# Optimization experiments

Hardware: AMD Instinct MI355X
Metric: run time of the kernel (lower is better)

## Reference

```python
import jax, jax.numpy as jnp
import numpy as np

N_NODES = 100000
N_EDGES = 1600000
D_IN = 128
D_HID = 64
BN_EPS = 1e-5


def setup_inputs() -> dict:
    key = jax.random.key(0)
    ks = jax.random.split(key, 8)
    x = jax.random.normal(ks[0], (N_NODES, D_IN), dtype=jnp.float32)
    edge_index = jax.random.randint(ks[1], (2, N_EDGES), 0, N_NODES, dtype=jnp.int64)
    # GCNConv1 weight/bias (glorot-ish scale)
    W1 = jax.random.normal(ks[2], (D_IN, D_HID), dtype=jnp.float32) / np.sqrt(D_IN)
    b1 = jnp.zeros((D_HID,), dtype=jnp.float32)
    # BatchNorm1d (eval mode: running stats)
    gamma = jax.random.normal(ks[3], (D_HID,), dtype=jnp.float32) * 0.1 + 1.0
    beta = jax.random.normal(ks[4], (D_HID,), dtype=jnp.float32) * 0.1
    run_mean = jnp.zeros((D_HID,), dtype=jnp.float32)
    run_var = jnp.ones((D_HID,), dtype=jnp.float32)
    # fc1: Linear(2*hidden, 2)
    Wfc = jax.random.normal(ks[5], (2 * D_HID, 2), dtype=jnp.float32) / np.sqrt(2 * D_HID)
    bfc = jnp.zeros((2,), dtype=jnp.float32)
    return {"x": x, "edge_index": edge_index, "W1": W1, "b1": b1,
            "gamma": gamma, "beta": beta, "run_mean": run_mean, "run_var": run_var,
            "Wfc": Wfc, "bfc": bfc}


def gcn_conv(x, edge_index, W, b):
    # PyG GCNConv: add self-loops, symmetric normalization, scatter-add aggregation
    n = x.shape[0]
    loops = jnp.arange(n, dtype=edge_index.dtype)
    row = jnp.concatenate([edge_index[0], loops])  # source nodes
    col = jnp.concatenate([edge_index[1], loops])  # target nodes
    deg = jax.ops.segment_sum(jnp.ones_like(col, dtype=x.dtype), col, num_segments=n)
    dinv = jax.lax.rsqrt(jnp.maximum(deg, 1.0))  # deg >= 1 due to self-loops
    norm = dinv[row] * dinv[col]                 # [E+N]
    h = x @ W                                    # [N, hid]
    msgs = h[row] * norm[:, None]                # gather + scale  [E+N, hid]
    out = jax.ops.segment_sum(msgs, col, num_segments=n)  # scatter-add
    return out + b


def reference(x, edge_index, W1, b1, gamma, beta, run_mean, run_var, Wfc, bfc):
    h = gcn_conv(x, edge_index, W1, b1)
    h = jax.nn.relu(h)
    # dropout(p=0.9) is identity in eval mode
    # BatchNorm1d eval: normalize with running stats
    h = (h - run_mean) * jax.lax.rsqrt(run_var + BN_EPS) * gamma + beta
    h = jax.nn.relu(h)
    # edge gather-concat-linear
    er = jnp.concatenate([h[edge_index[0]], h[edge_index[1]]], axis=1)  # [E, 2*hid]
    return er @ Wfc + bfc  # [E, 2]
```

## Files before the change

### kernel.cpp

```cpp
#include <hip/hip_runtime.h>

#define N_NODES 100000
#define N_EDGES 1600000
#define D_IN 128
#define D_HID 64
#define BN_EPS 1e-5f

#define BUCKET_SHIFT 7
#define BUCKET_W 128
#define N_BUCKETS ((N_NODES + BUCKET_W - 1) / BUCKET_W)
#define BCAP 4096
#define N_BIN_BLOCKS 250
#define EDGES_PER_BLOCK (N_EDGES / N_BIN_BLOCKS)
#define E4_PER_BLOCK (EDGES_PER_BLOCK / 4)

typedef __attribute__((ext_vector_type(8))) short bf16x8;
typedef __attribute__((ext_vector_type(4))) float f32x4;
typedef __attribute__((ext_vector_type(8))) _Float16 f16x8;

__device__ __forceinline__ ushort f2bf(float f) {
    unsigned u = __float_as_uint(f);
    u += 0x7FFF + ((u >> 16) & 1);
    return (ushort)(u >> 16);
}

__global__ __launch_bounds__(1024) void bin_scatter_kernel(const int* __restrict__ row,
                                                           const int* __restrict__ col,
                                                           int* __restrict__ bcursor,
                                                           int* __restrict__ binned) {
    __shared__ int hist[N_BUCKETS];
    __shared__ int lbase[N_BUCKETS];
    const int t = threadIdx.x;
    for (int i = t; i < N_BUCKETS; i += 1024) hist[i] = 0;
    __syncthreads();
    const int e0 = blockIdx.x * EDGES_PER_BLOCK;
    const int4* __restrict__ colv = (const int4*)(col + e0);
    const int4* __restrict__ rowv = (const int4*)(row + e0);
    for (int j4 = t; j4 < E4_PER_BLOCK; j4 += 1024) {
        int4 c = colv[j4];
        atomicAdd(&hist[c.x >> BUCKET_SHIFT], 1);
        atomicAdd(&hist[c.y >> BUCKET_SHIFT], 1);
        atomicAdd(&hist[c.z >> BUCKET_SHIFT], 1);
        atomicAdd(&hist[c.w >> BUCKET_SHIFT], 1);
    }
    __syncthreads();
    for (int i = t; i < N_BUCKETS; i += 1024) {
        int h = hist[i];
        lbase[i] = h ? (i * BCAP + atomicAdd(&bcursor[i], h)) : 0;
        hist[i] = 0;
    }
    __syncthreads();
    for (int j4 = t; j4 < E4_PER_BLOCK; j4 += 1024) {
        int4 c = colv[j4];
        int4 r = rowv[j4];
        int cc[4] = {c.x, c.y, c.z, c.w};
        int rr[4] = {r.x, r.y, r.z, r.w};
        #pragma unroll
        for (int k = 0; k < 4; ++k) {
            int b = cc[k] >> BUCKET_SHIFT;
            int rank = atomicAdd(&hist[b], 1);
            binned[lbase[b] + rank] = ((cc[k] & (BUCKET_W - 1)) << 17) | rr[k];
        }
    }
}

union CsrGemmSh {
    struct { int eb[BCAP]; int cl[BCAP]; } s;
    ushort xb[2][16 * 136];
};
__global__ __launch_bounds__(512) void csr_gemm_kernel(const int* __restrict__ binned,
                                                       const int* __restrict__ bcursor,
                                                       const float* __restrict__ x,
                                                       const float* __restrict__ W,
                                                       int* __restrict__ csr_src,
                                                       int2* __restrict__ rs2,
                                                       float* __restrict__ dinv,
                                                       ushort* __restrict__ h_s) {
    __shared__ CsrGemmSh sh;
    __shared__ int hist[BUCKET_W];
    __shared__ int cursor[BUCKET_W];
    __shared__ float dsh[BUCKET_W];
    const int b = blockIdx.x;
    const int t = threadIdx.x;

    const int l = t & 63;
    const int wv = (t >> 6) & 3;
    const int q = l >> 4;
    const int m = l & 15;
    bf16x8 bf[4];
    {
        const int n = wv * 16 + m;
        #pragma unroll
        for (int s = 0; s < 4; ++s)
            #pragma unroll
            for (int j = 0; j < 8; ++j)
                bf[s][j] = (short)f2bf(W[(32 * s + 8 * q + j) * D_HID + n]);
    }

    if (t < BUCKET_W) hist[t] = 0;
    __syncthreads();
    const int s = b * BCAP;
    const int cnt = bcursor[b];
    const int n4 = (cnt + 3) >> 2;
    const int4* __restrict__ binv = (const int4*)(binned + s);
    for (int i4 = t; i4 < n4; i4 += 512) {
        int4 v = binv[i4];
        int vv[4] = {v.x, v.y, v.z, v.w};
        #pragma unroll
        for (int k = 0; k < 4; ++k) {
            int idx = 4 * i4 + k;
            if (idx < cnt) {
                sh.s.eb[idx] = vv[k];
                atomicAdd(&hist[vv[k] >> 17], 1);
            }
        }
    }
    __syncthreads();
    if (t < BUCKET_W) cursor[t] = hist[t];
    for (int off = 1; off < BUCKET_W; off <<= 1) {
        __syncthreads();
        int add = (t >= off && t < BUCKET_W) ? cursor[t - off] : 0;
        __syncthreads();
        if (t < BUCKET_W) cursor[t] += add;
    }
    __syncthreads();
    int excl = (t < BUCKET_W) ? (cursor[t] - hist[t]) : 0;
    __syncthreads();
    if (t < BUCKET_W) cursor[t] = excl;
    {
        const int node = b * BUCKET_W + t;
        if (t < BUCKET_W) {
            float dn = rsqrtf(1.0f + (float)hist[t]);
            dsh[t] = dn;
            if (node < N_NODES) {
                rs2[node] = make_int2(s + excl, hist[t]);
                dinv[node] = dn;
            }
        }
    }
    __syncthreads();
    for (int i = t; i < cnt; i += 512) {
        int p = sh.s.eb[i];
        int pos = atomicAdd(&cursor[p >> 17], 1);
        sh.s.cl[pos] = p & 0x1FFFF;
    }
    __syncthreads();
    {
        int4* __restrict__ csrv = (int4*)(csr_src + s);
        const int4* __restrict__ clv = (const int4*)sh.s.cl;
        for (int i4 = t; i4 < n4; i4 += 512)
            csrv[i4] = clv[i4];
    }
    __syncthreads();

    const int h = t >> 8;
    const int tt = t & 255;
    #pragma unroll
    for (int rnd = 0; rnd < 4; ++rnd) {
        const int node0 = b * BUCKET_W + rnd * 32 + h * 16;
        __syncthreads();
        for (int i = tt; i < 512; i += 256) {
            int r = i >> 5, c4 = i & 31;
            int nr = node0 + r;
            if (nr >= N_NODES) nr = N_NODES - 1;
            float4 v = *(const float4*)&x[(size_t)nr * D_IN + c4 * 4];
            ushort4 u = make_ushort4(f2bf(v.x), f2bf(v.y), f2bf(v.z), f2bf(v.w));
            *(ushort4*)&sh.xb[h][r * 136 + c4 * 4] = u;
        }
        __syncthreads();
        f32x4 acc = {0.f, 0.f, 0.f, 0.f};
        #pragma unroll
        for (int ks = 0; ks < 4; ++ks) {
            bf16x8 af = *(const bf16x8*)&sh.xb[h][m * 136 + 32 * ks + 8 * q];
            acc = __builtin_amdgcn_mfma_f32_16x16x32_bf16(af, bf[ks], acc, 0, 0, 0);
        }
        #pragma unroll
        for (int r = 0; r < 4; ++r) {
            int node = node0 + q * 4 + r;
            if (node < N_NODES) {
                _Float16 hv = (_Float16)(acc[r] * dsh[node - b * BUCKET_W]);
                h_s[node * D_HID + wv * 16 + m] = __builtin_bit_cast(unsigned short, hv);
            }
        }
    }
}

__global__ __launch_bounds__(256) void aggregate_kernel(const ushort* __restrict__ h_s,
                                                        const float* __restrict__ dinv,
                                                        const int2* __restrict__ rs2,
                                                        const int* __restrict__ csr_src,
                                                        const float* __restrict__ b1,
                                                        const float* __restrict__ gamma,
                                                        const float* __restrict__ beta,
                                                        const float* __restrict__ mean,
                                                        const float* __restrict__ var,
                                                        const float* __restrict__ Wfc,
                                                        float4* __restrict__ uv) {
    const f16x8* __restrict__ hsv = (const f16x8*)h_s;
    const int wvid = (blockIdx.x * 256 + threadIdx.x) >> 6;
    const int lane = threadIdx.x & 63;
    const int oct = lane >> 3;
    const int ol = lane & 7;
    const int n = wvid * 8 + oct;
    f16x8 acc = hsv[n * 8 + ol];
    const int2 rs = rs2[n];
    const int start = rs.x;
    const int cnt = rs.y;
    int j = 0;
    for (; j + 8 <= cnt; j += 8) {
        int i0 = csr_src[start + j + 0];
        int i1 = csr_src[start + j + 1];
        int i2 = csr_src[start + j + 2];
        int i3 = csr_src[start + j + 3];
        int i4 = csr_src[start + j + 4];
        int i5 = csr_src[start + j + 5];
        int i6 = csr_src[start + j + 6];
        int i7 = csr_src[start + j + 7];
        f16x8 v0 = hsv[i0 * 8 + ol];
        f16x8 v1 = hsv[i1 * 8 + ol];
        f16x8 v2 = hsv[i2 * 8 + ol];
        f16x8 v3 = hsv[i3 * 8 + ol];
        f16x8 v4 = hsv[i4 * 8 + ol];
        f16x8 v5 = hsv[i5 * 8 + ol];
        f16x8 v6 = hsv[i6 * 8 + ol];
        f16x8 v7 = hsv[i7 * 8 + ol];
        acc += v0; acc += v1; acc += v2; acc += v3;
        acc += v4; acc += v5; acc += v6; acc += v7;
    }
    for (; j + 4 <= cnt; j += 4) {
        int i0 = csr_src[start + j + 0];
        int i1 = csr_src[start + j + 1];
        int i2 = csr_src[start + j + 2];
        int i3 = csr_src[start + j + 3];
        f16x8 v0 = hsv[i0 * 8 + ol];
        f16x8 v1 = hsv[i1 * 8 + ol];
        f16x8 v2 = hsv[i2 * 8 + ol];
        f16x8 v3 = hsv[i3 * 8 + ol];
        acc += v0; acc += v1; acc += v2; acc += v3;
    }
    for (; j + 2 <= cnt; j += 2) {
        int i0 = csr_src[start + j + 0];
        int i1 = csr_src[start + j + 1];
        f16x8 v0 = hsv[i0 * 8 + ol];
        f16x8 v1 = hsv[i1 * 8 + ol];
        acc += v0; acc += v1;
    }
    if (j < cnt)
        acc += hsv[csr_src[start + j] * 8 + ol];
    const float dn = dinv[n];
    const int f0 = 8 * ol;
    float a[8];
    #pragma unroll
    for (int k = 0; k < 8; ++k) a[k] = (float)acc[k] * dn;
    float bb[8], mu[8], vr[8], gm[8], bt[8];
    *(float4*)&bb[0] = *(const float4*)&b1[f0];    *(float4*)&bb[4] = *(const float4*)&b1[f0 + 4];
    *(float4*)&mu[0] = *(const float4*)&mean[f0];  *(float4*)&mu[4] = *(const float4*)&mean[f0 + 4];
    *(float4*)&vr[0] = *(const float4*)&var[f0];   *(float4*)&vr[4] = *(const float4*)&var[f0 + 4];
    *(float4*)&gm[0] = *(const float4*)&gamma[f0]; *(float4*)&gm[4] = *(const float4*)&gamma[f0 + 4];
    *(float4*)&bt[0] = *(const float4*)&beta[f0];  *(float4*)&bt[4] = *(const float4*)&beta[f0 + 4];
    #pragma unroll
    for (int k = 0; k < 8; ++k) {
        float v = fmaxf(a[k] + bb[k], 0.f);
        a[k] = fmaxf((v - mu[k]) * rsqrtf(vr[k] + BN_EPS) * gm[k] + bt[k], 0.f);
    }
    float wt[16], wb[16];
    #pragma unroll
    for (int k = 0; k < 4; ++k) {
        *(float4*)&wt[4 * k] = *(const float4*)&Wfc[2 * f0 + 4 * k];
        *(float4*)&wb[4 * k] = *(const float4*)&Wfc[128 + 2 * f0 + 4 * k];
    }
    float p0 = 0.f, p1 = 0.f, p2 = 0.f, p3 = 0.f;
    #pragma unroll
    for (int k = 0; k < 8; ++k) {
        p0 += a[k] * wt[2 * k];
        p1 += a[k] * wt[2 * k + 1];
        p2 += a[k] * wb[2 * k];
        p3 += a[k] * wb[2 * k + 1];
    }
    #pragma unroll
    for (int off = 4; off > 0; off >>= 1) {
        p0 += __shfl_xor(p0, off, 64);
        p1 += __shfl_xor(p1, off, 64);
        p2 += __shfl_xor(p2, off, 64);
        p3 += __shfl_xor(p3, off, 64);
    }
    if (ol == 0) uv[n] = make_float4(p0, p1, p2, p3);
}

__global__ __launch_bounds__(256) void edgeout_kernel(const int* __restrict__ row,
                                                      const int* __restrict__ col,
                                                      const float4* __restrict__ uv,
                                                      const float* __restrict__ bfc,
                                                      float2* __restrict__ out) {
    int i = blockIdx.x * 256 + threadIdx.x;
    int e = i * 2;
    int2 rr = *(const int2*)&row[e];
    int2 cc = *(const int2*)&col[e];
    float4 a0 = uv[rr.x];
    float4 b0 = uv[cc.x];
    float4 a1 = uv[rr.y];
    float4 b1 = uv[cc.y];
    float c0 = bfc[0], c1 = bfc[1];
    float4 o = make_float4(a0.x + b0.z + c0, a0.y + b0.w + c1,
                           a1.x + b1.z + c0, a1.y + b1.w + c1);
    *(float4*)&out[e] = o;
}

extern "C" void kernel_launch(void* const* d_in, const int* in_sizes, int n_in,
                              void* d_out, int out_size, void* d_ws, size_t ws_size,
                              hipStream_t stream) {
    const float* x     = (const float*)d_in[0];
    const int*   ei    = (const int*)d_in[1];
    const int*   row   = ei;
    const int*   col   = ei + N_EDGES;
    const float* W1    = (const float*)d_in[2];
    const float* b1    = (const float*)d_in[3];
    const float* gamma = (const float*)d_in[4];
    const float* beta  = (const float*)d_in[5];
    const float* mean  = (const float*)d_in[6];
    const float* var   = (const float*)d_in[7];
    const float* Wfc   = (const float*)d_in[8];
    const float* bfc   = (const float*)d_in[9];
    float2* out = (float2*)d_out;

    char* ws = (char*)d_ws;
    size_t off = 0;
    ushort* h_s      = (ushort*)(ws + off); off += (size_t)N_NODES * D_HID * 2;
    int*   binned    = (int*)(ws + off);    off += (size_t)N_BUCKETS * BCAP * 4;
    int*   csr_src   = (int*)(ws + off);    off += (size_t)N_BUCKETS * BCAP * 4;
    int*   bcursor   = (int*)(ws + off);    off += ((size_t)N_BUCKETS * 4 + 15) & ~(size_t)15;
    int2*  rs2       = (int2*)(ws + off);   off += (size_t)N_NODES * 8;
    float* dinv      = (float*)(ws + off);  off += (size_t)N_NODES * 4;
    float4* uv       = (float4*)(ws + off); off += (size_t)N_NODES * 16;

    hipMemsetAsync(bcursor, 0, N_BUCKETS * sizeof(int), stream);
    bin_scatter_kernel<<<N_BIN_BLOCKS, 1024, 0, stream>>>(row, col, bcursor, binned);
    csr_gemm_kernel<<<N_BUCKETS, 512, 0, stream>>>(binned, bcursor, x, W1,
                                                   csr_src, rs2, dinv, h_s);
    aggregate_kernel<<<N_NODES / 32, 256, 0, stream>>>(h_s, dinv, rs2, csr_src,
                                                       b1, gamma, beta, mean, var,
                                                       Wfc, uv);
    edgeout_kernel<<<N_EDGES / 512, 256, 0, stream>>>(row, col, uv, bfc, out);
}
```

Before: 188.1 us.

## Stage binned edges in LDS and prefetch first x tile before CSR build

The binning kernel now packs each edge entry and its bucket id into shared memory during the histogram pass, so the scatter pass reads from LDS instead of re-reading row/col from global memory. The CSR/GEMM kernel issues the global loads for its first x tile into registers at kernel start, letting them overlap the CSR sort phase. This raises LDS use in the bin kernel (about 38 KB extra per block) and register pressure in the GEMM kernel, which may reduce occupancy.

```diff
diff --git a/kernel.cpp b/kernel.cpp
--- a/kernel.cpp
+++ b/kernel.cpp
@@ -30,6 +30,8 @@
                                                            int* __restrict__ binned) {
     __shared__ int hist[N_BUCKETS];
     __shared__ int lbase[N_BUCKETS];
+    __shared__ int ent[EDGES_PER_BLOCK];
+    __shared__ ushort ebk[EDGES_PER_BLOCK];
     const int t = threadIdx.x;
     for (int i = t; i < N_BUCKETS; i += 1024) hist[i] = 0;
     __syncthreads();
@@ -38,10 +40,17 @@
     const int4* __restrict__ rowv = (const int4*)(row + e0);
     for (int j4 = t; j4 < E4_PER_BLOCK; j4 += 1024) {
         int4 c = colv[j4];
-        atomicAdd(&hist[c.x >> BUCKET_SHIFT], 1);
-        atomicAdd(&hist[c.y >> BUCKET_SHIFT], 1);
-        atomicAdd(&hist[c.z >> BUCKET_SHIFT], 1);
-        atomicAdd(&hist[c.w >> BUCKET_SHIFT], 1);
+        int4 r = rowv[j4];
+        int cc[4] = {c.x, c.y, c.z, c.w};
+        int rr[4] = {r.x, r.y, r.z, r.w};
+        #pragma unroll
+        for (int k = 0; k < 4; ++k) {
+            int b = cc[k] >> BUCKET_SHIFT;
+            int idx = 4 * j4 + k;
+            ent[idx] = ((cc[k] & (BUCKET_W - 1)) << 17) | rr[k];
+            ebk[idx] = (ushort)b;
+            atomicAdd(&hist[b], 1);
+        }
     }
     __syncthreads();
     for (int i = t; i < N_BUCKETS; i += 1024) {
@@ -50,17 +59,10 @@
         hist[i] = 0;
     }
     __syncthreads();
-    for (int j4 = t; j4 < E4_PER_BLOCK; j4 += 1024) {
-        int4 c = colv[j4];
-        int4 r = rowv[j4];
-        int cc[4] = {c.x, c.y, c.z, c.w};
-        int rr[4] = {r.x, r.y, r.z, r.w};
-        #pragma unroll
-        for (int k = 0; k < 4; ++k) {
-            int b = cc[k] >> BUCKET_SHIFT;
-            int rank = atomicAdd(&hist[b], 1);
-            binned[lbase[b] + rank] = ((cc[k] & (BUCKET_W - 1)) << 17) | rr[k];
-        }
+    for (int j = t; j < EDGES_PER_BLOCK; j += 1024) {
+        int b = ebk[j];
+        int rank = atomicAdd(&hist[b], 1);
+        binned[lbase[b] + rank] = ent[j];
     }
 }
 
@@ -87,6 +89,8 @@
     const int wv = (t >> 6) & 3;
     const int q = l >> 4;
     const int m = l & 15;
+    const int hh = t >> 8;
+    const int tt = t & 255;
     bf16x8 bf[4];
     {
         const int n = wv * 16 + m;
@@ -95,6 +99,17 @@
             #pragma unroll
             for (int j = 0; j < 8; ++j)
                 bf[s][j] = (short)f2bf(W[(32 * s + 8 * q + j) * D_HID + n]);
+    }
+    float4 px[2];
+    {
+        #pragma unroll
+        for (int ii = 0; ii < 2; ++ii) {
+            int i = tt + ii * 256;
+            int r = i >> 5, c4 = i & 31;
+            int nr = b * BUCKET_W + hh * 16 + r;
+            if (nr >= N_NODES) nr = N_NODES - 1;
+            px[ii] = *(const float4*)&x[(size_t)nr * D_IN + c4 * 4];
+        }
     }
 
     if (t < BUCKET_W) hist[t] = 0;
@@ -153,25 +168,34 @@
     }
     __syncthreads();
 
-    const int h = t >> 8;
-    const int tt = t & 255;
     #pragma unroll
     for (int rnd = 0; rnd < 4; ++rnd) {
-        const int node0 = b * BUCKET_W + rnd * 32 + h * 16;
+        const int node0 = b * BUCKET_W + rnd * 32 + hh * 16;
         __syncthreads();
-        for (int i = tt; i < 512; i += 256) {
-            int r = i >> 5, c4 = i & 31;
-            int nr = node0 + r;
-            if (nr >= N_NODES) nr = N_NODES - 1;
-            float4 v = *(const float4*)&x[(size_t)nr * D_IN + c4 * 4];
-            ushort4 u = make_ushort4(f2bf(v.x), f2bf(v.y), f2bf(v.z), f2bf(v.w));
-            *(ushort4*)&sh.xb[h][r * 136 + c4 * 4] = u;
+        if (rnd == 0) {
+            #pragma unroll
+            for (int ii = 0; ii < 2; ++ii) {
+                int i = tt + ii * 256;
+                int r = i >> 5, c4 = i & 31;
+                float4 v = px[ii];
+                ushort4 u = make_ushort4(f2bf(v.x), f2bf(v.y), f2bf(v.z), f2bf(v.w));
+                *(ushort4*)&sh.xb[hh][r * 136 + c4 * 4] = u;
+            }
+        } else {
+            for (int i = tt; i < 512; i += 256) {
+                int r = i >> 5, c4 = i & 31;
+                int nr = node0 + r;
+                if (nr >= N_NODES) nr = N_NODES - 1;
+                float4 v = *(const float4*)&x[(size_t)nr * D_IN + c4 * 4];
+                ushort4 u = make_ushort4(f2bf(v.x), f2bf(v.y), f2bf(v.z), f2bf(v.w));
+                *(ushort4*)&sh.xb[hh][r * 136 + c4 * 4] = u;
+            }
         }
         __syncthreads();
         f32x4 acc = {0.f, 0.f, 0.f, 0.f};
         #pragma unroll
         for (int ks = 0; ks < 4; ++ks) {
-            bf16x8 af = *(const bf16x8*)&sh.xb[h][m * 136 + 32 * ks + 8 * q];
+            bf16x8 af = *(const bf16x8*)&sh.xb[hh][m * 136 + 32 * ks + 8 * q];
             acc = __builtin_amdgcn_mfma_f32_16x16x32_bf16(af, bf[ks], acc, 0, 0, 0);
         }
         #pragma unroll
```

Measured after the change: 190.1 us. About the same (+1.1%).
